# Optimization experiments

Measured on AMD Instinct MI355X. Metric: run time of the kernel, lower is better.

Reference implementation:

```python
import jax, jax.numpy as jnp
import numpy as np

B, S, IN, H, BB, M = 256, 512, 64, 256, 256, 64


def _lecun_tanh(x):
    return 1.7159 * jnp.tanh(0.666 * x)


def setup_inputs() -> dict:
    key = jax.random.key(0)
    ks = jax.random.split(key, 32)
    def g(i, shape, fan_in):
        return jax.random.normal(ks[i], shape, jnp.float32) * (fan_in ** -0.5)
    return {
        "x": jax.random.normal(ks[0], (B, S, IN), jnp.float32),
        "timespans": jax.random.uniform(ks[1], (B, S), jnp.float32, minval=0.01, maxval=1.0),
        "hx": jnp.zeros((B, H), jnp.float32),
        # CfC cell backbone (2 layers, lecun_tanh)
        "bb_w0": g(2, (IN + H, BB), IN + H), "bb_b0": jnp.zeros((BB,), jnp.float32),
        "bb_w1": g(3, (BB, BB), BB), "bb_b1": jnp.zeros((BB,), jnp.float32),
        # CfC heads ff1/ff2/time_a/time_b
        "ff1_w": g(4, (BB, H), BB), "ff1_b": jnp.zeros((H,), jnp.float32),
        "ff2_w": g(5, (BB, H), BB), "ff2_b": jnp.zeros((H,), jnp.float32),
        "ta_w": g(6, (BB, H), BB), "ta_b": jnp.zeros((H,), jnp.float32),
        "tb_w": g(7, (BB, H), BB), "tb_b": jnp.zeros((H,), jnp.float32),
        # projection hidden -> motor
        "proj_w": g(8, (H, M), H), "proj_b": jnp.zeros((M,), jnp.float32),
        # intensity head: M->16 SiLU ->3 Softplus
        "ih_w0": g(9, (M, 16), M), "ih_b0": jnp.zeros((16,), jnp.float32),
        "ih_w1": g(10, (16, 3), 16), "ih_b1": jnp.zeros((3,), jnp.float32),
        # action head: M->16 SiLU ->1 Tanh
        "ah_w0": g(11, (M, 16), M), "ah_b0": jnp.zeros((16,), jnp.float32),
        "ah_w1": g(12, (16, 1), 16), "ah_b1": jnp.zeros((1,), jnp.float32),
        # confidence head: M->8 SiLU ->1 Sigmoid
        "ch_w0": g(13, (M, 8), M), "ch_b0": jnp.zeros((8,), jnp.float32),
        "ch_w1": g(14, (8, 1), 8), "ch_b1": jnp.zeros((1,), jnp.float32),
    }


def reference(x, timespans, hx, bb_w0, bb_b0, bb_w1, bb_b1, ff1_w, ff1_b, ff2_w, ff2_b,
              ta_w, ta_b, tb_w, tb_b, proj_w, proj_b,
              ih_w0, ih_b0, ih_w1, ih_b1, ah_w0, ah_b0, ah_w1, ah_b1,
              ch_w0, ch_b0, ch_w1, ch_b1):
    ts = timespans[..., None]  # (B,S,1)

    def step(h, inp):
        x_t, ts_t = inp  # (B,IN), (B,1)
        z = jnp.concatenate([x_t, h], axis=-1)
        z = _lecun_tanh(z @ bb_w0 + bb_b0)
        z = _lecun_tanh(z @ bb_w1 + bb_b1)
        ff1 = jnp.tanh(z @ ff1_w + ff1_b)
        ff2 = jnp.tanh(z @ ff2_w + ff2_b)
        t_interp = jax.nn.sigmoid((z @ ta_w + ta_b) * ts_t + (z @ tb_w + tb_b))
        h_new = ff1 * (1.0 - t_interp) + t_interp * ff2
        return h_new, h_new

    xs = (jnp.swapaxes(x, 0, 1), jnp.swapaxes(ts, 0, 1))  # time-major
    h_n, h_seq = jax.lax.scan(step, hx, xs)               # h_seq: (S,B,H)
    cfc = jnp.swapaxes(h_seq, 0, 1) @ proj_w + proj_b     # (B,S,M)
    intensities = jax.nn.softplus(jax.nn.silu(cfc @ ih_w0 + ih_b0) @ ih_w1 + ih_b1)
    actions = jnp.tanh(jax.nn.silu(cfc @ ah_w0 + ah_b0) @ ah_w1 + ah_b1)
    confidence = jax.nn.sigmoid(jax.nn.silu(cfc @ ch_w0 + ch_b0) @ ch_w1 + ch_b1)
    return intensities, actions, confidence, h_n
```

## Files before the change

### kernel.cpp

```cpp
#include <hip/hip_runtime.h>
#include <hip/hip_bf16.h>

#define BN  256
#define SN  512
#define INN 64
#define HN  256
#define MN  64

#define ZINS 328
#define ZBS  264
#define CFS  72
#define HTS  36

#define OFF_ACT  393216
#define OFF_CONF 524288
#define OFF_HN   655360

#define FLAG_STRIDE 32
#define FLAG_BYTES  16384

typedef _Float16 h8 __attribute__((ext_vector_type(8)));
typedef float fx4 __attribute__((ext_vector_type(4)));
typedef unsigned long long u64;

union h4u {
    _Float16 h[4];
    u64 u;
};

__device__ __forceinline__ fx4 mfma16(h8 a, h8 b, fx4 c) {
    return __builtin_amdgcn_mfma_f32_16x16x32_f16(a, b, c, 0, 0, 0);
}
__device__ __forceinline__ float fast_tanh(float x) {
    float e = __expf(2.0f * x);
    return 1.0f - 2.0f / (e + 1.0f);
}
__device__ __forceinline__ float fast_sig(float x) { return 1.0f / (1.0f + __expf(-x)); }
__device__ __forceinline__ float lecun_tanh(float x) { return 1.7159f * fast_tanh(0.666f * x); }
__device__ __forceinline__ float softplus_f(float x) {
    return fmaxf(x, 0.0f) + __logf(1.0f + __expf(-fabsf(x)));
}

template <int NW>
__device__ __forceinline__ h8 loadB(const float* __restrict__ w, int col, int kbase) {
    h8 r;
#pragma unroll
    for (int j = 0; j < 8; ++j) r[j] = (_Float16)w[(kbase + j) * NW + col];
    return r;
}

__global__ void __launch_bounds__(512, 1) lh_scan_kernel(
    const float* __restrict__ x, const float* __restrict__ tsp, const float* __restrict__ hx,
    const float* __restrict__ w0, const float* __restrict__ b0,
    const float* __restrict__ w1, const float* __restrict__ b1,
    const float* __restrict__ f1w, const float* __restrict__ f1b,
    const float* __restrict__ f2w, const float* __restrict__ f2b,
    const float* __restrict__ taw, const float* __restrict__ tab,
    const float* __restrict__ tbw, const float* __restrict__ tbb,
    const float* __restrict__ pw, const float* __restrict__ pbias,
    const float* __restrict__ ihw0, const float* __restrict__ ihb0,
    const float* __restrict__ ihw1, const float* __restrict__ ihb1,
    const float* __restrict__ ahw0, const float* __restrict__ ahb0,
    const float* __restrict__ ahw1, const float* __restrict__ ahb1,
    const float* __restrict__ chw0, const float* __restrict__ chb0,
    const float* __restrict__ chw1, const float* __restrict__ chb1,
    float* __restrict__ out, unsigned int* __restrict__ flags,
    u64* __restrict__ hbuf)
{
    __shared__ __align__(16) _Float16 zin[16 * ZINS];
    __shared__ __align__(16) _Float16 z0b[16 * ZBS];
    __shared__ __align__(16) _Float16 z1b[16 * ZBS];
    __shared__ __align__(16) _Float16 cfcb[16 * CFS];
    __shared__ __align__(16) _Float16 pfl[8 * 4 * 64 * 8];
    __shared__ __align__(16) _Float16 w1l[8 * 8 * 64 * 8];
    __shared__ __align__(16) float htmp[4 * 16 * HTS];
    __shared__ float hidI[16 * 16];
    __shared__ float hidA[16 * 16];
    __shared__ float hidC[16 * 8];
    __shared__ float tsb[2][16];
    __shared__ float wsm[80];

    const int tid  = threadIdx.x;
    const int wv   = tid >> 6;
    const int lane = tid & 63;
    const int lo   = lane & 15;
    const int hi   = lane >> 4;
    const int hi8  = hi * 8;

    const int bid   = blockIdx.x;
    const int xcd   = bid & 7;
    const int c     = (bid >> 3) & 7;
    const int gsel  = bid >> 6;
    const int g     = xcd + 8 * gsel;
    const int bg    = g * 16;
    const int sbase = c * 32;

    if (tid < 48)          wsm[tid] = ihw1[tid];
    else if (tid < 51)     wsm[tid] = ihb1[tid - 48];
    else if (tid < 67)     wsm[tid] = ahw1[tid - 51];
    else if (tid == 67)    wsm[67]  = ahb1[0];
    else if (tid < 76)     wsm[tid] = chw1[tid - 68];
    else if (tid == 76)    wsm[76]  = chb1[0];

    {
        int r = tid >> 5, c8 = (tid & 31) * 8;
#pragma unroll
        for (int j = 0; j < 8; ++j)
            zin[r * ZINS + 64 + c8 + j] = (_Float16)hx[(bg + r) * HN + c8 + j];
        int c2 = (tid & 31) * 2;
        const float* xp = &x[((size_t)(bg + r) * SN + 0) * INN + c2];
        zin[r * ZINS + c2]     = (_Float16)xp[0];
        zin[r * ZINS + c2 + 1] = (_Float16)xp[1];
    }
    if (tid < 16) tsb[0][tid] = tsp[(bg + tid) * SN + 0];

    const int cg0 = wv, cg1 = wv + 8;
    const float b00 = b0[cg0 * 16 + lo], b01 = b0[cg1 * 16 + lo];
    const float b10 = b1[cg0 * 16 + lo], b11 = b1[cg1 * 16 + lo];

    const int hm  = wv >> 1;
    const int hcol = sbase + (wv & 1) * 16 + lo;
    const float* hwp = (hm == 0) ? f1w : (hm == 1) ? f2w : (hm == 2) ? taw : tbw;
    const float* hbp = (hm == 0) ? f1b : (hm == 1) ? f2b : (hm == 2) ? tab : tbb;
    const float hb = hbp[hcol];

    h8 w0f0[10], w0f1[10], w1f0[8], hdf[8];
#pragma unroll
    for (int kk = 0; kk < 10; ++kk) {
        w0f0[kk] = loadB<256>(w0, cg0 * 16 + lo, kk * 32 + hi8);
        w0f1[kk] = loadB<256>(w0, cg1 * 16 + lo, kk * 32 + hi8);
    }
#pragma unroll
    for (int kk = 0; kk < 8; ++kk) {
        w1f0[kk] = loadB<256>(w1, cg0 * 16 + lo, kk * 32 + hi8);
        hdf[kk]  = loadB<256>(hwp, hcol, kk * 32 + hi8);
        h8 f = loadB<256>(w1, cg1 * 16 + lo, kk * 32 + hi8);
        *(h8*)&w1l[((kk * 8 + wv) * 64 + lane) * 8] = f;
    }
    float pbv = 0.0f;
    if (wv < 4) {
        pbv = pbias[wv * 16 + lo];
#pragma unroll
        for (int kk = 0; kk < 8; ++kk) {
            h8 f = loadB<64>(pw, wv * 16 + lo, kk * 32 + hi8);
            *(h8*)&pfl[((kk * 4 + wv) * 64 + lane) * 8] = f;
        }
    }
    h8 hwf[2] = {};
    float hbv = 0.0f;
    if (wv == 4) {
        hbv = ihb0[lo];
#pragma unroll
        for (int kk = 0; kk < 2; ++kk) hwf[kk] = loadB<16>(ihw0, lo, kk * 32 + hi8);
    } else if (wv == 5) {
        hbv = ahb0[lo];
#pragma unroll
        for (int kk = 0; kk < 2; ++kk) hwf[kk] = loadB<16>(ahw0, lo, kk * 32 + hi8);
    } else if (wv == 6) {
        int cc = (lo < 8) ? lo : 0;
        hbv = (lo < 8) ? chb0[lo] : 0.0f;
#pragma unroll
        for (int kk = 0; kk < 2; ++kk) hwf[kk] = loadB<8>(chw0, cc, kk * 32 + hi8);
    }

    __syncthreads();

    for (int t = 0; t <= SN; ++t) {
        const int pr = t & 7;

        if (t < SN) {
            fx4 a0 = {b00, b00, b00, b00}, a1 = {b01, b01, b01, b01};
#pragma unroll
            for (int kk = 0; kk < 10; ++kk) {
                h8 a = *(const h8*)&zin[lo * ZINS + kk * 32 + hi8];
                a0 = mfma16(a, w0f0[kk], a0);
                a1 = mfma16(a, w0f1[kk], a1);
            }
#pragma unroll
            for (int i = 0; i < 4; ++i) {
                int r = hi * 4 + i;
                z0b[r * ZBS + cg0 * 16 + lo] = (_Float16)lecun_tanh(a0[i]);
                z0b[r * ZBS + cg1 * 16 + lo] = (_Float16)lecun_tanh(a1[i]);
            }
        }
        __syncthreads();

        if (t + 1 < SN) {
            int r = tid >> 5, c2 = (tid & 31) * 2;
            const float* xp = &x[((size_t)(bg + r) * SN + (t + 1)) * INN + c2];
            zin[r * ZINS + c2]     = (_Float16)xp[0];
            zin[r * ZINS + c2 + 1] = (_Float16)xp[1];
            if (tid < 16) tsb[(t + 1) & 1][tid] = tsp[(bg + tid) * SN + t + 1];
        }

        if (t < SN) {
            fx4 a0 = {b10, b10, b10, b10}, a1 = {b11, b11, b11, b11};
#pragma unroll
            for (int kk = 0; kk < 8; ++kk) {
                h8 a = *(const h8*)&z0b[lo * ZBS + kk * 32 + hi8];
                h8 b1f = *(const h8*)&w1l[((kk * 8 + wv) * 64 + lane) * 8];
                a0 = mfma16(a, w1f0[kk], a0);
                a1 = mfma16(a, b1f, a1);
            }
#pragma unroll
            for (int i = 0; i < 4; ++i) {
                int r = hi * 4 + i;
                z1b[r * ZBS + cg0 * 16 + lo] = (_Float16)lecun_tanh(a0[i]);
                z1b[r * ZBS + cg1 * 16 + lo] = (_Float16)lecun_tanh(a1[i]);
            }
        }
        __syncthreads();

        if (t < SN) {
            fx4 acc = {hb, hb, hb, hb};
#pragma unroll
            for (int kk = 0; kk < 8; ++kk) {
                h8 a = *(const h8*)&z1b[lo * ZBS + kk * 32 + hi8];
                acc = mfma16(a, hdf[kk], acc);
            }
#pragma unroll
            for (int i = 0; i < 4; ++i)
                htmp[(hm * 16 + hi * 4 + i) * HTS + (wv & 1) * 16 + lo] = acc[i];
        }
        __syncthreads();

        if (t < SN && tid < 128) {
            int r = tid >> 3, c4 = (tid & 7) * 4;
            h4u pk;
            float hn3 = 0.0f;
#pragma unroll
            for (int k = 0; k < 4; ++k) {
                float a1v = htmp[(0 * 16 + r) * HTS + c4 + k];
                float a2v = htmp[(1 * 16 + r) * HTS + c4 + k];
                float a3v = htmp[(2 * 16 + r) * HTS + c4 + k];
                float a4v = htmp[(3 * 16 + r) * HTS + c4 + k];
                float tv  = tsb[t & 1][r];
                float ff1 = fast_tanh(a1v);
                float ff2 = fast_tanh(a2v);
                float ti  = fast_sig(a3v * tv + a4v);
                float hn  = ff1 + ti * (ff2 - ff1);
                pk.h[k] = (_Float16)hn;
                if (t == SN - 1) out[OFF_HN + (bg + r) * HN + sbase + c4 + k] = hn;
                hn3 = hn;
            }
            (void)hn3;
            size_t idx = ((((size_t)((t + 1) & 1) * 16 + g) * 16) + r) * 64 + (sbase + c4) / 4;
            __hip_atomic_store(&hbuf[idx], pk.u, __ATOMIC_RELAXED, __HIP_MEMORY_SCOPE_AGENT);
        }
        __syncthreads();
        if (t < SN && tid == 0)
            __hip_atomic_store(&flags[(g * 8 + c) * FLAG_STRIDE], (unsigned)(t + 1),
                               __ATOMIC_RELAXED, __HIP_MEMORY_SCOPE_AGENT);

        if (t >= 1 && c == pr && wv < 4) {
            fx4 acc = {pbv, pbv, pbv, pbv};
#pragma unroll
            for (int kk = 0; kk < 8; ++kk) {
                h8 a = *(const h8*)&zin[lo * ZINS + 64 + kk * 32 + hi8];
                h8 b = *(const h8*)&pfl[((kk * 4 + wv) * 64 + lane) * 8];
                acc = mfma16(a, b, acc);
            }
#pragma unroll
            for (int i = 0; i < 4; ++i)
                cfcb[(hi * 4 + i) * CFS + wv * 16 + lo] = (_Float16)acc[i];
        }
        __syncthreads();

        if (t >= 1 && c == pr && wv >= 4 && wv < 7) {
            fx4 acc = {hbv, hbv, hbv, hbv};
#pragma unroll
            for (int kk = 0; kk < 2; ++kk) {
                h8 a = *(const h8*)&cfcb[lo * CFS + kk * 32 + hi8];
                acc = mfma16(a, hwf[kk], acc);
            }
#pragma unroll
            for (int i = 0; i < 4; ++i) {
                float v = acc[i];
                v = v * fast_sig(v);
                int r = hi * 4 + i;
                if (wv == 4)       hidI[r * 16 + lo] = v;
                else if (wv == 5)  hidA[r * 16 + lo] = v;
                else if (lo < 8)   hidC[r * 8 + lo]  = v;
            }
        }
        __syncthreads();

        if (t >= 1 && c == pr && tid < 80) {
            int r = tid / 5, o = tid % 5;
            int tc = t - 1;
            int b = bg + r;
            if (o < 3) {
                float s = wsm[48 + o];
#pragma unroll
                for (int u = 0; u < 16; ++u) s += hidI[r * 16 + u] * wsm[u * 3 + o];
                out[(size_t)(b * SN + tc) * 3 + o] = softplus_f(s);
            } else if (o == 3) {
                float s = wsm[67];
#pragma unroll
                for (int u = 0; u < 16; ++u) s += hidA[r * 16 + u] * wsm[51 + u];
                out[OFF_ACT + b * SN + tc] = fast_tanh(s);
            } else {
                float s = wsm[76];
#pragma unroll
                for (int u = 0; u < 8; ++u) s += hidC[r * 8 + u] * wsm[68 + u];
                out[OFF_CONF + b * SN + tc] = fast_sig(s);
            }
        }

        if (t < SN) {
            if (tid < 8) {
                unsigned target = (unsigned)(t + 1);
                while (__hip_atomic_load(&flags[(g * 8 + tid) * FLAG_STRIDE],
                                         __ATOMIC_RELAXED, __HIP_MEMORY_SCOPE_AGENT) < target) {}
            }
            __syncthreads();
            {
                int r = tid >> 5, c8 = (tid & 31) * 8;
                size_t idx = ((((size_t)((t + 1) & 1) * 16 + g) * 16) + r) * 64 + c8 / 4;
                u64 v0 = __hip_atomic_load(&hbuf[idx],     __ATOMIC_RELAXED, __HIP_MEMORY_SCOPE_AGENT);
                u64 v1 = __hip_atomic_load(&hbuf[idx + 1], __ATOMIC_RELAXED, __HIP_MEMORY_SCOPE_AGENT);
                *(u64*)&zin[r * ZINS + 64 + c8]     = v0;
                *(u64*)&zin[r * ZINS + 64 + c8 + 4] = v1;
            }
        }
        __syncthreads();
    }
}

extern "C" void kernel_launch(void* const* d_in, const int* in_sizes, int n_in,
                              void* d_out, int out_size, void* d_ws, size_t ws_size,
                              hipStream_t stream) {
    (void)in_sizes; (void)n_in; (void)out_size; (void)ws_size;
    const float* p[29];
    for (int i = 0; i < 29; ++i) p[i] = (const float*)d_in[i];
    unsigned int* flags = (unsigned int*)d_ws;
    u64* hbuf = (u64*)((char*)d_ws + FLAG_BYTES);
    hipMemsetAsync(d_ws, 0, FLAG_BYTES, stream);
    hipLaunchKernelGGL(lh_scan_kernel, dim3(128), dim3(512), 0, stream,
        p[0], p[1], p[2], p[3], p[4], p[5], p[6], p[7], p[8], p[9], p[10], p[11], p[12],
        p[13], p[14], p[15], p[16], p[17], p[18], p[19], p[20], p[21], p[22], p[23],
        p[24], p[25], p[26], p[27], p[28], (float*)d_out, flags, hbuf);
}
```

Before: 2.325 ms.

## Double block to 1024 threads, one column group per wave, overlap projection

```diff
diff --git a/kernel.cpp b/kernel.cpp
--- a/kernel.cpp
+++ b/kernel.cpp
@@ -22,11 +22,7 @@
 typedef _Float16 h8 __attribute__((ext_vector_type(8)));
 typedef float fx4 __attribute__((ext_vector_type(4)));
 typedef unsigned long long u64;
-
-union h4u {
-    _Float16 h[4];
-    u64 u;
-};
+union h4u { _Float16 h[4]; u64 u; };
 
 __device__ __forceinline__ fx4 mfma16(h8 a, h8 b, fx4 c) {
     return __builtin_amdgcn_mfma_f32_16x16x32_f16(a, b, c, 0, 0, 0);
@@ -49,7 +45,7 @@
     return r;
 }
 
-__global__ void __launch_bounds__(512, 1) lh_scan_kernel(
+__global__ void __launch_bounds__(1024, 1) lh_scan_kernel(
     const float* __restrict__ x, const float* __restrict__ tsp, const float* __restrict__ hx,
     const float* __restrict__ w0, const float* __restrict__ b0,
     const float* __restrict__ w1, const float* __restrict__ b1,
@@ -71,8 +67,8 @@
     __shared__ __align__(16) _Float16 z0b[16 * ZBS];
     __shared__ __align__(16) _Float16 z1b[16 * ZBS];
     __shared__ __align__(16) _Float16 cfcb[16 * CFS];
+    __shared__ __align__(16) _Float16 hdl[8 * 8 * 64 * 8];
     __shared__ __align__(16) _Float16 pfl[8 * 4 * 64 * 8];
-    __shared__ __align__(16) _Float16 w1l[8 * 8 * 64 * 8];
     __shared__ __align__(16) float htmp[4 * 16 * HTS];
     __shared__ float hidI[16 * 16];
     __shared__ float hidA[16 * 16];
@@ -102,7 +98,7 @@
     else if (tid < 76)     wsm[tid] = chw1[tid - 68];
     else if (tid == 76)    wsm[76]  = chb1[0];
 
-    {
+    if (tid < 512) {
         int r = tid >> 5, c8 = (tid & 31) * 8;
 #pragma unroll
         for (int j = 0; j < 8; ++j)
@@ -114,49 +110,49 @@
     }
     if (tid < 16) tsb[0][tid] = tsp[(bg + tid) * SN + 0];
 
-    const int cg0 = wv, cg1 = wv + 8;
-    const float b00 = b0[cg0 * 16 + lo], b01 = b0[cg1 * 16 + lo];
-    const float b10 = b1[cg0 * 16 + lo], b11 = b1[cg1 * 16 + lo];
-
-    const int hm  = wv >> 1;
+    const float b0v = b0[wv * 16 + lo];
+    const float b1v = b1[wv * 16 + lo];
+
+    h8 w0f[10], w1f[8];
+#pragma unroll
+    for (int kk = 0; kk < 10; ++kk) w0f[kk] = loadB<256>(w0, wv * 16 + lo, kk * 32 + hi8);
+#pragma unroll
+    for (int kk = 0; kk < 8; ++kk)  w1f[kk] = loadB<256>(w1, wv * 16 + lo, kk * 32 + hi8);
+
+    const int hm   = wv >> 1;
     const int hcol = sbase + (wv & 1) * 16 + lo;
-    const float* hwp = (hm == 0) ? f1w : (hm == 1) ? f2w : (hm == 2) ? taw : tbw;
-    const float* hbp = (hm == 0) ? f1b : (hm == 1) ? f2b : (hm == 2) ? tab : tbb;
-    const float hb = hbp[hcol];
-
-    h8 w0f0[10], w0f1[10], w1f0[8], hdf[8];
-#pragma unroll
-    for (int kk = 0; kk < 10; ++kk) {
-        w0f0[kk] = loadB<256>(w0, cg0 * 16 + lo, kk * 32 + hi8);
-        w0f1[kk] = loadB<256>(w0, cg1 * 16 + lo, kk * 32 + hi8);
-    }
-#pragma unroll
-    for (int kk = 0; kk < 8; ++kk) {
-        w1f0[kk] = loadB<256>(w1, cg0 * 16 + lo, kk * 32 + hi8);
-        hdf[kk]  = loadB<256>(hwp, hcol, kk * 32 + hi8);
-        h8 f = loadB<256>(w1, cg1 * 16 + lo, kk * 32 + hi8);
-        *(h8*)&w1l[((kk * 8 + wv) * 64 + lane) * 8] = f;
+    float hb = 0.0f;
+    if (wv < 8) {
+        const float* hwp = (hm == 0) ? f1w : (hm == 1) ? f2w : (hm == 2) ? taw : tbw;
+        const float* hbp = (hm == 0) ? f1b : (hm == 1) ? f2b : (hm == 2) ? tab : tbb;
+        hb = hbp[hcol];
+#pragma unroll
+        for (int kk = 0; kk < 8; ++kk) {
+            h8 f = loadB<256>(hwp, hcol, kk * 32 + hi8);
+            *(h8*)&hdl[((wv * 8 + kk) * 64 + lane) * 8] = f;
+        }
     }
     float pbv = 0.0f;
-    if (wv < 4) {
-        pbv = pbias[wv * 16 + lo];
+    if (wv >= 8 && wv < 12) {
+        int u = wv - 8;
+        pbv = pbias[u * 16 + lo];
 #pragma unroll
         for (int kk = 0; kk < 8; ++kk) {
-            h8 f = loadB<64>(pw, wv * 16 + lo, kk * 32 + hi8);
-            *(h8*)&pfl[((kk * 4 + wv) * 64 + lane) * 8] = f;
+            h8 f = loadB<64>(pw, u * 16 + lo, kk * 32 + hi8);
+            *(h8*)&pfl[((kk * 4 + u) * 64 + lane) * 8] = f;
         }
     }
     h8 hwf[2] = {};
     float hbv = 0.0f;
-    if (wv == 4) {
+    if (wv == 12) {
         hbv = ihb0[lo];
 #pragma unroll
         for (int kk = 0; kk < 2; ++kk) hwf[kk] = loadB<16>(ihw0, lo, kk * 32 + hi8);
-    } else if (wv == 5) {
+    } else if (wv == 13) {
         hbv = ahb0[lo];
 #pragma unroll
         for (int kk = 0; kk < 2; ++kk) hwf[kk] = loadB<16>(ahw0, lo, kk * 32 + hi8);
-    } else if (wv == 6) {
+    } else if (wv == 14) {
         int cc = (lo < 8) ? lo : 0;
         hbv = (lo < 8) ? chb0[lo] : 0.0f;
 #pragma unroll
@@ -169,23 +165,19 @@
         const int pr = t & 7;
 
         if (t < SN) {
-            fx4 a0 = {b00, b00, b00, b00}, a1 = {b01, b01, b01, b01};
+            fx4 acc = {b0v, b0v, b0v, b0v};
 #pragma unroll
             for (int kk = 0; kk < 10; ++kk) {
                 h8 a = *(const h8*)&zin[lo * ZINS + kk * 32 + hi8];
-                a0 = mfma16(a, w0f0[kk], a0);
-                a1 = mfma16(a, w0f1[kk], a1);
-            }
-#pragma unroll
-            for (int i = 0; i < 4; ++i) {
-                int r = hi * 4 + i;
-                z0b[r * ZBS + cg0 * 16 + lo] = (_Float16)lecun_tanh(a0[i]);
-                z0b[r * ZBS + cg1 * 16 + lo] = (_Float16)lecun_tanh(a1[i]);
-            }
-        }
-        __syncthreads();
-
-        if (t + 1 < SN) {
+                acc = mfma16(a, w0f[kk], acc);
+            }
+#pragma unroll
+            for (int i = 0; i < 4; ++i)
+                z0b[(hi * 4 + i) * ZBS + wv * 16 + lo] = (_Float16)lecun_tanh(acc[i]);
+        }
+        __syncthreads();
+
+        if (t + 1 < SN && tid < 512) {
             int r = tid >> 5, c2 = (tid & 31) * 2;
             const float* xp = &x[((size_t)(bg + r) * SN + (t + 1)) * INN + c2];
             zin[r * ZINS + c2]     = (_Float16)xp[0];
@@ -194,40 +186,48 @@
         }
 
         if (t < SN) {
-            fx4 a0 = {b10, b10, b10, b10}, a1 = {b11, b11, b11, b11};
+            fx4 acc = {b1v, b1v, b1v, b1v};
 #pragma unroll
             for (int kk = 0; kk < 8; ++kk) {
                 h8 a = *(const h8*)&z0b[lo * ZBS + kk * 32 + hi8];
-                h8 b1f = *(const h8*)&w1l[((kk * 8 + wv) * 64 + lane) * 8];
-                a0 = mfma16(a, w1f0[kk], a0);
-                a1 = mfma16(a, b1f, a1);
-            }
-#pragma unroll
-            for (int i = 0; i < 4; ++i) {
-                int r = hi * 4 + i;
-                z1b[r * ZBS + cg0 * 16 + lo] = (_Float16)lecun_tanh(a0[i]);
-                z1b[r * ZBS + cg1 * 16 + lo] = (_Float16)lecun_tanh(a1[i]);
-            }
-        }
-        __syncthreads();
-
-        if (t < SN) {
+                acc = mfma16(a, w1f[kk], acc);
+            }
+#pragma unroll
+            for (int i = 0; i < 4; ++i)
+                z1b[(hi * 4 + i) * ZBS + wv * 16 + lo] = (_Float16)lecun_tanh(acc[i]);
+        }
+        __syncthreads();
+
+        if (t < SN && wv < 8) {
             fx4 acc = {hb, hb, hb, hb};
 #pragma unroll
             for (int kk = 0; kk < 8; ++kk) {
                 h8 a = *(const h8*)&z1b[lo * ZBS + kk * 32 + hi8];
-                acc = mfma16(a, hdf[kk], acc);
+                h8 b = *(const h8*)&hdl[((wv * 8 + kk) * 64 + lane) * 8];
+                acc = mfma16(a, b, acc);
             }
 #pragma unroll
             for (int i = 0; i < 4; ++i)
                 htmp[(hm * 16 + hi * 4 + i) * HTS + (wv & 1) * 16 + lo] = acc[i];
+        }
+        if (t >= 1 && c == pr && wv >= 8 && wv < 12) {
+            int u = wv - 8;
+            fx4 acc = {pbv, pbv, pbv, pbv};
+#pragma unroll
+            for (int kk = 0; kk < 8; ++kk) {
+                h8 a = *(const h8*)&zin[lo * ZINS + 64 + kk * 32 + hi8];
+                h8 b = *(const h8*)&pfl[((kk * 4 + u) * 64 + lane) * 8];
+                acc = mfma16(a, b, acc);
+            }
+#pragma unroll
+            for (int i = 0; i < 4; ++i)
+                cfcb[(hi * 4 + i) * CFS + u * 16 + lo] = (_Float16)acc[i];
         }
         __syncthreads();
 
         if (t < SN && tid < 128) {
             int r = tid >> 3, c4 = (tid & 7) * 4;
             h4u pk;
-            float hn3 = 0.0f;
 #pragma unroll
             for (int k = 0; k < 4; ++k) {
                 float a1v = htmp[(0 * 16 + r) * HTS + c4 + k];
@@ -241,32 +241,11 @@
                 float hn  = ff1 + ti * (ff2 - ff1);
                 pk.h[k] = (_Float16)hn;
                 if (t == SN - 1) out[OFF_HN + (bg + r) * HN + sbase + c4 + k] = hn;
-                hn3 = hn;
-            }
-            (void)hn3;
-            size_t idx = ((((size_t)((t + 1) & 1) * 16 + g) * 16) + r) * 64 + (sbase + c4) / 4;
+            }
+            size_t idx = (((size_t)((t + 1) & 1) * 256) + g * 16 + r) * 64 + (sbase + c4) / 4;
             __hip_atomic_store(&hbuf[idx], pk.u, __ATOMIC_RELAXED, __HIP_MEMORY_SCOPE_AGENT);
         }
-        __syncthreads();
-        if (t < SN && tid == 0)
-            __hip_atomic_store(&flags[(g * 8 + c) * FLAG_STRIDE], (unsigned)(t + 1),
-                               __ATOMIC_RELAXED, __HIP_MEMORY_SCOPE_AGENT);
-
-        if (t >= 1 && c == pr && wv < 4) {
-            fx4 acc = {pbv, pbv, pbv, pbv};
-#pragma unroll
-            for (int kk = 0; kk < 8; ++kk) {
-                h8 a = *(const h8*)&zin[lo * ZINS + 64 + kk * 32 + hi8];
-                h8 b = *(const h8*)&pfl[((kk * 4 + wv) * 64 + lane) * 8];
-                acc = mfma16(a, b, acc);
-            }
-#pragma unroll
-            for (int i = 0; i < 4; ++i)
-                cfcb[(hi * 4 + i) * CFS + wv * 16 + lo] = (_Float16)acc[i];
-        }
-        __syncthreads();
-
-        if (t >= 1 && c == pr && wv >= 4 && wv < 7) {
+        if (t >= 1 && c == pr && wv >= 12 && wv < 15) {
             fx4 acc = {hbv, hbv, hbv, hbv};
 #pragma unroll
             for (int kk = 0; kk < 2; ++kk) {
@@ -278,15 +257,19 @@
                 float v = acc[i];
                 v = v * fast_sig(v);
                 int r = hi * 4 + i;
-                if (wv == 4)       hidI[r * 16 + lo] = v;
-                else if (wv == 5)  hidA[r * 16 + lo] = v;
+                if (wv == 12)      hidI[r * 16 + lo] = v;
+                else if (wv == 13) hidA[r * 16 + lo] = v;
                 else if (lo < 8)   hidC[r * 8 + lo]  = v;
             }
         }
         __syncthreads();
-
-        if (t >= 1 && c == pr && tid < 80) {
-            int r = tid / 5, o = tid % 5;
+        if (t < SN && tid == 0)
+            __hip_atomic_store(&flags[(g * 8 + c) * FLAG_STRIDE], (unsigned)(t + 1),
+                               __ATOMIC_RELAXED, __HIP_MEMORY_SCOPE_AGENT);
+
+        if (t >= 1 && c == pr && tid >= 512 && tid < 592) {
+            int local = tid - 512;
+            int r = local / 5, o = local % 5;
             int tc = t - 1;
             int b = bg + r;
             if (o < 3) {
@@ -306,7 +289,6 @@
                 out[OFF_CONF + b * SN + tc] = fast_sig(s);
             }
         }
-
         if (t < SN) {
             if (tid < 8) {
                 unsigned target = (unsigned)(t + 1);
@@ -314,9 +296,9 @@
                                          __ATOMIC_RELAXED, __HIP_MEMORY_SCOPE_AGENT) < target) {}
             }
             __syncthreads();
-            {
+            if (tid < 512) {
                 int r = tid >> 5, c8 = (tid & 31) * 8;
-                size_t idx = ((((size_t)((t + 1) & 1) * 16 + g) * 16) + r) * 64 + c8 / 4;
+                size_t idx = (((size_t)((t + 1) & 1) * 256) + g * 16 + r) * 64 + c8 / 4;
                 u64 v0 = __hip_atomic_load(&hbuf[idx],     __ATOMIC_RELAXED, __HIP_MEMORY_SCOPE_AGENT);
                 u64 v1 = __hip_atomic_load(&hbuf[idx + 1], __ATOMIC_RELAXED, __HIP_MEMORY_SCOPE_AGENT);
                 *(u64*)&zin[r * ZINS + 64 + c8]     = v0;
@@ -336,7 +318,7 @@
     unsigned int* flags = (unsigned int*)d_ws;
     u64* hbuf = (u64*)((char*)d_ws + FLAG_BYTES);
     hipMemsetAsync(d_ws, 0, FLAG_BYTES, stream);
-    hipLaunchKernelGGL(lh_scan_kernel, dim3(128), dim3(512), 0, stream,
+    hipLaunchKernelGGL(lh_scan_kernel, dim3(128), dim3(1024), 0, stream,
         p[0], p[1], p[2], p[3], p[4], p[5], p[6], p[7], p[8], p[9], p[10], p[11], p[12],
         p[13], p[14], p[15], p[16], p[17], p[18], p[19], p[20], p[21], p[22], p[23],
         p[24], p[25], p[26], p[27], p[28], (float*)d_out, flags, hbuf);
```

Measured after the change: 3.125 ms. 1.34x slower.

## Halve block to four waves, keep all weights in registers, merge step barriers

Applied to the files above, without the earlier changes.

```diff
diff --git a/kernel.cpp b/kernel.cpp
--- a/kernel.cpp
+++ b/kernel.cpp
@@ -22,11 +22,7 @@
 typedef _Float16 h8 __attribute__((ext_vector_type(8)));
 typedef float fx4 __attribute__((ext_vector_type(4)));
 typedef unsigned long long u64;
-
-union h4u {
-    _Float16 h[4];
-    u64 u;
-};
+union h4u { _Float16 h[4]; u64 u; };
 
 __device__ __forceinline__ fx4 mfma16(h8 a, h8 b, fx4 c) {
     return __builtin_amdgcn_mfma_f32_16x16x32_f16(a, b, c, 0, 0, 0);
@@ -49,7 +45,7 @@
     return r;
 }
 
-__global__ void __launch_bounds__(512, 1) lh_scan_kernel(
+__global__ void __launch_bounds__(256, 1) lh_scan_kernel(
     const float* __restrict__ x, const float* __restrict__ tsp, const float* __restrict__ hx,
     const float* __restrict__ w0, const float* __restrict__ b0,
     const float* __restrict__ w1, const float* __restrict__ b1,
@@ -72,7 +68,6 @@
     __shared__ __align__(16) _Float16 z1b[16 * ZBS];
     __shared__ __align__(16) _Float16 cfcb[16 * CFS];
     __shared__ __align__(16) _Float16 pfl[8 * 4 * 64 * 8];
-    __shared__ __align__(16) _Float16 w1l[8 * 8 * 64 * 8];
     __shared__ __align__(16) float htmp[4 * 16 * HTS];
     __shared__ float hidI[16 * 16];
     __shared__ float hidA[16 * 16];
@@ -103,60 +98,69 @@
     else if (tid == 76)    wsm[76]  = chb1[0];
 
     {
-        int r = tid >> 5, c8 = (tid & 31) * 8;
-#pragma unroll
-        for (int j = 0; j < 8; ++j)
-            zin[r * ZINS + 64 + c8 + j] = (_Float16)hx[(bg + r) * HN + c8 + j];
-        int c2 = (tid & 31) * 2;
-        const float* xp = &x[((size_t)(bg + r) * SN + 0) * INN + c2];
-        zin[r * ZINS + c2]     = (_Float16)xp[0];
-        zin[r * ZINS + c2 + 1] = (_Float16)xp[1];
+        int r = tid >> 4, c16 = (tid & 15) * 16;
+#pragma unroll
+        for (int j = 0; j < 16; ++j)
+            zin[r * ZINS + 64 + c16 + j] = (_Float16)hx[(bg + r) * HN + c16 + j];
+        int c4 = (tid & 15) * 4;
+        fx4 xv = *(const fx4*)&x[((size_t)(bg + r) * SN + 0) * INN + c4];
+        h4u pk;
+#pragma unroll
+        for (int j = 0; j < 4; ++j) pk.h[j] = (_Float16)xv[j];
+        *(u64*)&zin[r * ZINS + c4] = pk.u;
     }
     if (tid < 16) tsb[0][tid] = tsp[(bg + tid) * SN + 0];
 
-    const int cg0 = wv, cg1 = wv + 8;
-    const float b00 = b0[cg0 * 16 + lo], b01 = b0[cg1 * 16 + lo];
-    const float b10 = b1[cg0 * 16 + lo], b11 = b1[cg1 * 16 + lo];
-
-    const int hm  = wv >> 1;
-    const int hcol = sbase + (wv & 1) * 16 + lo;
-    const float* hwp = (hm == 0) ? f1w : (hm == 1) ? f2w : (hm == 2) ? taw : tbw;
-    const float* hbp = (hm == 0) ? f1b : (hm == 1) ? f2b : (hm == 2) ? tab : tbb;
-    const float hb = hbp[hcol];
-
-    h8 w0f0[10], w0f1[10], w1f0[8], hdf[8];
-#pragma unroll
-    for (int kk = 0; kk < 10; ++kk) {
-        w0f0[kk] = loadB<256>(w0, cg0 * 16 + lo, kk * 32 + hi8);
-        w0f1[kk] = loadB<256>(w0, cg1 * 16 + lo, kk * 32 + hi8);
-    }
-#pragma unroll
-    for (int kk = 0; kk < 8; ++kk) {
-        w1f0[kk] = loadB<256>(w1, cg0 * 16 + lo, kk * 32 + hi8);
-        hdf[kk]  = loadB<256>(hwp, hcol, kk * 32 + hi8);
-        h8 f = loadB<256>(w1, cg1 * 16 + lo, kk * 32 + hi8);
-        *(h8*)&w1l[((kk * 8 + wv) * 64 + lane) * 8] = f;
-    }
-    float pbv = 0.0f;
-    if (wv < 4) {
-        pbv = pbias[wv * 16 + lo];
+    float b0v[4], b1v[4];
+#pragma unroll
+    for (int q = 0; q < 4; ++q) {
+        b0v[q] = b0[(wv * 4 + q) * 16 + lo];
+        b1v[q] = b1[(wv * 4 + q) * 16 + lo];
+    }
+
+    const float* hwp = (wv == 0) ? f1w : (wv == 1) ? f2w : (wv == 2) ? taw : tbw;
+    const float* hbp = (wv == 0) ? f1b : (wv == 1) ? f2b : (wv == 2) ? tab : tbb;
+    float hbs[2] = { hbp[sbase + lo], hbp[sbase + 16 + lo] };
+
+    h8 w0f[4][10], w1f[4][8], hdf[2][8];
+#pragma unroll
+    for (int q = 0; q < 4; ++q) {
+#pragma unroll
+        for (int kk = 0; kk < 10; ++kk)
+            w0f[q][kk] = loadB<256>(w0, (wv * 4 + q) * 16 + lo, kk * 32 + hi8);
+#pragma unroll
+        for (int kk = 0; kk < 8; ++kk)
+            w1f[q][kk] = loadB<256>(w1, (wv * 4 + q) * 16 + lo, kk * 32 + hi8);
+    }
+#pragma unroll
+    for (int s = 0; s < 2; ++s)
+#pragma unroll
+        for (int kk = 0; kk < 8; ++kk)
+            hdf[s][kk] = loadB<256>(hwp, sbase + s * 16 + lo, kk * 32 + hi8);
+
+    {
 #pragma unroll
         for (int kk = 0; kk < 8; ++kk) {
             h8 f = loadB<64>(pw, wv * 16 + lo, kk * 32 + hi8);
             *(h8*)&pfl[((kk * 4 + wv) * 64 + lane) * 8] = f;
         }
     }
+    float pbv[2] = { 0.0f, 0.0f };
+    if (wv >= 2) {
+        pbv[0] = pbias[((wv - 2) * 2 + 0) * 16 + lo];
+        pbv[1] = pbias[((wv - 2) * 2 + 1) * 16 + lo];
+    }
     h8 hwf[2] = {};
     float hbv = 0.0f;
-    if (wv == 4) {
+    if (wv == 0) {
         hbv = ihb0[lo];
 #pragma unroll
         for (int kk = 0; kk < 2; ++kk) hwf[kk] = loadB<16>(ihw0, lo, kk * 32 + hi8);
-    } else if (wv == 5) {
+    } else if (wv == 1) {
         hbv = ahb0[lo];
 #pragma unroll
         for (int kk = 0; kk < 2; ++kk) hwf[kk] = loadB<16>(ahw0, lo, kk * 32 + hi8);
-    } else if (wv == 6) {
+    } else if (wv == 2) {
         int cc = (lo < 8) ? lo : 0;
         hbv = (lo < 8) ? chb0[lo] : 0.0f;
 #pragma unroll
@@ -169,104 +173,123 @@
         const int pr = t & 7;
 
         if (t < SN) {
-            fx4 a0 = {b00, b00, b00, b00}, a1 = {b01, b01, b01, b01};
+            fx4 a0 = {b0v[0], b0v[0], b0v[0], b0v[0]};
+            fx4 a1 = {b0v[1], b0v[1], b0v[1], b0v[1]};
+            fx4 a2 = {b0v[2], b0v[2], b0v[2], b0v[2]};
+            fx4 a3 = {b0v[3], b0v[3], b0v[3], b0v[3]};
 #pragma unroll
             for (int kk = 0; kk < 10; ++kk) {
                 h8 a = *(const h8*)&zin[lo * ZINS + kk * 32 + hi8];
-                a0 = mfma16(a, w0f0[kk], a0);
-                a1 = mfma16(a, w0f1[kk], a1);
+                a0 = mfma16(a, w0f[0][kk], a0);
+                a1 = mfma16(a, w0f[1][kk], a1);
+                a2 = mfma16(a, w0f[2][kk], a2);
+                a3 = mfma16(a, w0f[3][kk], a3);
             }
 #pragma unroll
             for (int i = 0; i < 4; ++i) {
                 int r = hi * 4 + i;
-                z0b[r * ZBS + cg0 * 16 + lo] = (_Float16)lecun_tanh(a0[i]);
-                z0b[r * ZBS + cg1 * 16 + lo] = (_Float16)lecun_tanh(a1[i]);
+                z0b[r * ZBS + (wv * 4 + 0) * 16 + lo] = (_Float16)lecun_tanh(a0[i]);
+                z0b[r * ZBS + (wv * 4 + 1) * 16 + lo] = (_Float16)lecun_tanh(a1[i]);
+                z0b[r * ZBS + (wv * 4 + 2) * 16 + lo] = (_Float16)lecun_tanh(a2[i]);
+                z0b[r * ZBS + (wv * 4 + 3) * 16 + lo] = (_Float16)lecun_tanh(a3[i]);
             }
         }
         __syncthreads();
 
         if (t + 1 < SN) {
-            int r = tid >> 5, c2 = (tid & 31) * 2;
-            const float* xp = &x[((size_t)(bg + r) * SN + (t + 1)) * INN + c2];
-            zin[r * ZINS + c2]     = (_Float16)xp[0];
-            zin[r * ZINS + c2 + 1] = (_Float16)xp[1];
+            int r = tid >> 4, c4 = (tid & 15) * 4;
+            fx4 xv = *(const fx4*)&x[((size_t)(bg + r) * SN + (t + 1)) * INN + c4];
+            h4u pk;
+#pragma unroll
+            for (int j = 0; j < 4; ++j) pk.h[j] = (_Float16)xv[j];
+            *(u64*)&zin[r * ZINS + c4] = pk.u;
             if (tid < 16) tsb[(t + 1) & 1][tid] = tsp[(bg + tid) * SN + t + 1];
         }
-
         if (t < SN) {
-            fx4 a0 = {b10, b10, b10, b10}, a1 = {b11, b11, b11, b11};
+            fx4 a0 = {b1v[0], b1v[0], b1v[0], b1v[0]};
+            fx4 a1 = {b1v[1], b1v[1], b1v[1], b1v[1]};
+            fx4 a2 = {b1v[2], b1v[2], b1v[2], b1v[2]};
+            fx4 a3 = {b1v[3], b1v[3], b1v[3], b1v[3]};
 #pragma unroll
             for (int kk = 0; kk < 8; ++kk) {
                 h8 a = *(const h8*)&z0b[lo * ZBS + kk * 32 + hi8];
-                h8 b1f = *(const h8*)&w1l[((kk * 8 + wv) * 64 + lane) * 8];
-                a0 = mfma16(a, w1f0[kk], a0);
-                a1 = mfma16(a, b1f, a1);
+                a0 = mfma16(a, w1f[0][kk], a0);
+                a1 = mfma16(a, w1f[1][kk], a1);
+                a2 = mfma16(a, w1f[2][kk], a2);
+                a3 = mfma16(a, w1f[3][kk], a3);
             }
 #pragma unroll
             for (int i = 0; i < 4; ++i) {
                 int r = hi * 4 + i;
-                z1b[r * ZBS + cg0 * 16 + lo] = (_Float16)lecun_tanh(a0[i]);
-                z1b[r * ZBS + cg1 * 16 + lo] = (_Float16)lecun_tanh(a1[i]);
+                z1b[r * ZBS + (wv * 4 + 0) * 16 + lo] = (_Float16)lecun_tanh(a0[i]);
+                z1b[r * ZBS + (wv * 4 + 1) * 16 + lo] = (_Float16)lecun_tanh(a1[i]);
+                z1b[r * ZBS + (wv * 4 + 2) * 16 + lo] = (_Float16)lecun_tanh(a2[i]);
+                z1b[r * ZBS + (wv * 4 + 3) * 16 + lo] = (_Float16)lecun_tanh(a3[i]);
             }
         }
         __syncthreads();
 
         if (t < SN) {
-            fx4 acc = {hb, hb, hb, hb};
+            fx4 a0 = {hbs[0], hbs[0], hbs[0], hbs[0]};
+            fx4 a1 = {hbs[1], hbs[1], hbs[1], hbs[1]};
 #pragma unroll
             for (int kk = 0; kk < 8; ++kk) {
                 h8 a = *(const h8*)&z1b[lo * ZBS + kk * 32 + hi8];
-                acc = mfma16(a, hdf[kk], acc);
-            }
-#pragma unroll
-            for (int i = 0; i < 4; ++i)
-                htmp[(hm * 16 + hi * 4 + i) * HTS + (wv & 1) * 16 + lo] = acc[i];
+                a0 = mfma16(a, hdf[0][kk], a0);
+                a1 = mfma16(a, hdf[1][kk], a1);
+            }
+#pragma unroll
+            for (int i = 0; i < 4; ++i) {
+                htmp[(wv * 16 + hi * 4 + i) * HTS + lo]      = a0[i];
+                htmp[(wv * 16 + hi * 4 + i) * HTS + 16 + lo] = a1[i];
+            }
         }
         __syncthreads();
 
         if (t < SN && tid < 128) {
             int r = tid >> 3, c4 = (tid & 7) * 4;
+            fx4 v0 = *(const fx4*)&htmp[(0 * 16 + r) * HTS + c4];
+            fx4 v1 = *(const fx4*)&htmp[(1 * 16 + r) * HTS + c4];
+            fx4 v2 = *(const fx4*)&htmp[(2 * 16 + r) * HTS + c4];
+            fx4 v3 = *(const fx4*)&htmp[(3 * 16 + r) * HTS + c4];
+            float tv = tsb[t & 1][r];
             h4u pk;
-            float hn3 = 0.0f;
 #pragma unroll
             for (int k = 0; k < 4; ++k) {
-                float a1v = htmp[(0 * 16 + r) * HTS + c4 + k];
-                float a2v = htmp[(1 * 16 + r) * HTS + c4 + k];
-                float a3v = htmp[(2 * 16 + r) * HTS + c4 + k];
-                float a4v = htmp[(3 * 16 + r) * HTS + c4 + k];
-                float tv  = tsb[t & 1][r];
-                float ff1 = fast_tanh(a1v);
-                float ff2 = fast_tanh(a2v);
-                float ti  = fast_sig(a3v * tv + a4v);
+                float ff1 = fast_tanh(v0[k]);
+                float ff2 = fast_tanh(v1[k]);
+                float ti  = fast_sig(v2[k] * tv + v3[k]);
                 float hn  = ff1 + ti * (ff2 - ff1);
                 pk.h[k] = (_Float16)hn;
                 if (t == SN - 1) out[OFF_HN + (bg + r) * HN + sbase + c4 + k] = hn;
-                hn3 = hn;
-            }
-            (void)hn3;
-            size_t idx = ((((size_t)((t + 1) & 1) * 16 + g) * 16) + r) * 64 + (sbase + c4) / 4;
+            }
+            size_t idx = (((size_t)((t + 1) & 1) * 256) + g * 16 + r) * 64 + (sbase + c4) / 4;
             __hip_atomic_store(&hbuf[idx], pk.u, __ATOMIC_RELAXED, __HIP_MEMORY_SCOPE_AGENT);
         }
-        __syncthreads();
-        if (t < SN && tid == 0)
-            __hip_atomic_store(&flags[(g * 8 + c) * FLAG_STRIDE], (unsigned)(t + 1),
-                               __ATOMIC_RELAXED, __HIP_MEMORY_SCOPE_AGENT);
-
-        if (t >= 1 && c == pr && wv < 4) {
-            fx4 acc = {pbv, pbv, pbv, pbv};
+        if (t >= 1 && c == pr && wv >= 2) {
+            fx4 a0 = {pbv[0], pbv[0], pbv[0], pbv[0]};
+            fx4 a1 = {pbv[1], pbv[1], pbv[1], pbv[1]};
+            int cg0 = (wv - 2) * 2, cg1 = cg0 + 1;
 #pragma unroll
             for (int kk = 0; kk < 8; ++kk) {
                 h8 a = *(const h8*)&zin[lo * ZINS + 64 + kk * 32 + hi8];
-                h8 b = *(const h8*)&pfl[((kk * 4 + wv) * 64 + lane) * 8];
-                acc = mfma16(a, b, acc);
-            }
-#pragma unroll
-            for (int i = 0; i < 4; ++i)
-                cfcb[(hi * 4 + i) * CFS + wv * 16 + lo] = (_Float16)acc[i];
-        }
-        __syncthreads();
-
-        if (t >= 1 && c == pr && wv >= 4 && wv < 7) {
+                h8 f0 = *(const h8*)&pfl[((kk * 4 + cg0) * 64 + lane) * 8];
+                h8 f1 = *(const h8*)&pfl[((kk * 4 + cg1) * 64 + lane) * 8];
+                a0 = mfma16(a, f0, a0);
+                a1 = mfma16(a, f1, a1);
+            }
+#pragma unroll
+            for (int i = 0; i < 4; ++i) {
+                cfcb[(hi * 4 + i) * CFS + cg0 * 16 + lo] = (_Float16)a0[i];
+                cfcb[(hi * 4 + i) * CFS + cg1 * 16 + lo] = (_Float16)a1[i];
+            }
+        }
+        __syncthreads();
+        if (t < SN && tid == 0)
+            __hip_atomic_store(&flags[(g * 8 + c) * FLAG_STRIDE], (unsigned)(t + 2),
+                               __ATOMIC_RELAXED, __HIP_MEMORY_SCOPE_AGENT);
+
+        if (t >= 1 && c == pr && wv < 3) {
             fx4 acc = {hbv, hbv, hbv, hbv};
 #pragma unroll
             for (int kk = 0; kk < 2; ++kk) {
@@ -278,49 +301,69 @@
                 float v = acc[i];
                 v = v * fast_sig(v);
                 int r = hi * 4 + i;
-                if (wv == 4)       hidI[r * 16 + lo] = v;
-                else if (wv == 5)  hidA[r * 16 + lo] = v;
+                if (wv == 0)       hidI[r * 16 + lo] = v;
+                else if (wv == 1)  hidA[r * 16 + lo] = v;
                 else if (lo < 8)   hidC[r * 8 + lo]  = v;
             }
         }
-        __syncthreads();
-
-        if (t >= 1 && c == pr && tid < 80) {
-            int r = tid / 5, o = tid % 5;
+        if (t < SN && wv == 3 && lane < 8) {
+            unsigned target = (unsigned)(t + 2);
+            while (__hip_atomic_load(&flags[(g * 8 + lane) * FLAG_STRIDE],
+                                     __ATOMIC_RELAXED, __HIP_MEMORY_SCOPE_AGENT) < target) {}
+        }
+        __syncthreads();
+
+        if (t < SN) {
+            int r = tid >> 4, cw = (tid & 15) * 16;
+            size_t idx = (((size_t)((t + 1) & 1) * 256) + g * 16 + r) * 64 + cw / 4;
+            u64 v0 = __hip_atomic_load(&hbuf[idx],     __ATOMIC_RELAXED, __HIP_MEMORY_SCOPE_AGENT);
+            u64 v1 = __hip_atomic_load(&hbuf[idx + 1], __ATOMIC_RELAXED, __HIP_MEMORY_SCOPE_AGENT);
+            u64 v2 = __hip_atomic_load(&hbuf[idx + 2], __ATOMIC_RELAXED, __HIP_MEMORY_SCOPE_AGENT);
+            u64 v3 = __hip_atomic_load(&hbuf[idx + 3], __ATOMIC_RELAXED, __HIP_MEMORY_SCOPE_AGENT);
+            if (t >= 1 && c == pr && tid < 80) {
+                int rr = tid / 5, o = tid % 5;
+                int tc = t - 1;
+                int b = bg + rr;
+                if (o < 3) {
+                    float s = wsm[48 + o];
+#pragma unroll
+                    for (int u = 0; u < 16; ++u) s += hidI[rr * 16 + u] * wsm[u * 3 + o];
+                    out[(size_t)(b * SN + tc) * 3 + o] = softplus_f(s);
+                } else if (o == 3) {
+                    float s = wsm[67];
+#pragma unroll
+                    for (int u = 0; u < 16; ++u) s += hidA[rr * 16 + u] * wsm[51 + u];
+                    out[OFF_ACT + b * SN + tc] = fast_tanh(s);
+                } else {
+                    float s = wsm[76];
+#pragma unroll
+                    for (int u = 0; u < 8; ++u) s += hidC[rr * 8 + u] * wsm[68 + u];
+                    out[OFF_CONF + b * SN + tc] = fast_sig(s);
+                }
+            }
+            *(u64*)&zin[r * ZINS + 64 + cw]      = v0;
+            *(u64*)&zin[r * ZINS + 64 + cw + 4]  = v1;
+            *(u64*)&zin[r * ZINS + 64 + cw + 8]  = v2;
+            *(u64*)&zin[r * ZINS + 64 + cw + 12] = v3;
+        } else if (t >= 1 && c == pr && tid < 80) {
+            int rr = tid / 5, o = tid % 5;
             int tc = t - 1;
-            int b = bg + r;
+            int b = bg + rr;
             if (o < 3) {
                 float s = wsm[48 + o];
 #pragma unroll
-                for (int u = 0; u < 16; ++u) s += hidI[r * 16 + u] * wsm[u * 3 + o];
+                for (int u = 0; u < 16; ++u) s += hidI[rr * 16 + u] * wsm[u * 3 + o];
                 out[(size_t)(b * SN + tc) * 3 + o] = softplus_f(s);
             } else if (o == 3) {
                 float s = wsm[67];
 #pragma unroll
-                for (int u = 0; u < 16; ++u) s += hidA[r * 16 + u] * wsm[51 + u];
+                for (int u = 0; u < 16; ++u) s += hidA[rr * 16 + u] * wsm[51 + u];
                 out[OFF_ACT + b * SN + tc] = fast_tanh(s);
             } else {
                 float s = wsm[76];
 #pragma unroll
-                for (int u = 0; u < 8; ++u) s += hidC[r * 8 + u] * wsm[68 + u];
+                for (int u = 0; u < 8; ++u) s += hidC[rr * 8 + u] * wsm[68 + u];
                 out[OFF_CONF + b * SN + tc] = fast_sig(s);
-            }
-        }
-
-        if (t < SN) {
-            if (tid < 8) {
-                unsigned target = (unsigned)(t + 1);
-                while (__hip_atomic_load(&flags[(g * 8 + tid) * FLAG_STRIDE],
-                                         __ATOMIC_RELAXED, __HIP_MEMORY_SCOPE_AGENT) < target) {}
-            }
-            __syncthreads();
-            {
-                int r = tid >> 5, c8 = (tid & 31) * 8;
-                size_t idx = ((((size_t)((t + 1) & 1) * 16 + g) * 16) + r) * 64 + c8 / 4;
-                u64 v0 = __hip_atomic_load(&hbuf[idx],     __ATOMIC_RELAXED, __HIP_MEMORY_SCOPE_AGENT);
-                u64 v1 = __hip_atomic_load(&hbuf[idx + 1], __ATOMIC_RELAXED, __HIP_MEMORY_SCOPE_AGENT);
-                *(u64*)&zin[r * ZINS + 64 + c8]     = v0;
-                *(u64*)&zin[r * ZINS + 64 + c8 + 4] = v1;
             }
         }
         __syncthreads();
@@ -336,7 +379,7 @@
     unsigned int* flags = (unsigned int*)d_ws;
     u64* hbuf = (u64*)((char*)d_ws + FLAG_BYTES);
     hipMemsetAsync(d_ws, 0, FLAG_BYTES, stream);
-    hipLaunchKernelGGL(lh_scan_kernel, dim3(128), dim3(512), 0, stream,
+    hipLaunchKernelGGL(lh_scan_kernel, dim3(128), dim3(256), 0, stream,
         p[0], p[1], p[2], p[3], p[4], p[5], p[6], p[7], p[8], p[9], p[10], p[11], p[12],
         p[13], p[14], p[15], p[16], p[17], p[18], p[19], p[20], p[21], p[22], p[23],
         p[24], p[25], p[26], p[27], p[28], (float*)d_out, flags, hbuf);
```

New measurement: 2.818 ms. +21.2%, slower.

## Cut barriers per step and overlap x-part GEMM with cross-block h exchange

Applied to the files above, without the earlier changes.

```diff
diff --git a/kernel.cpp b/kernel.cpp
--- a/kernel.cpp
+++ b/kernel.cpp
@@ -22,11 +22,7 @@
 typedef _Float16 h8 __attribute__((ext_vector_type(8)));
 typedef float fx4 __attribute__((ext_vector_type(4)));
 typedef unsigned long long u64;
-
-union h4u {
-    _Float16 h[4];
-    u64 u;
-};
+union h4u { _Float16 h[4]; u64 u; };
 
 __device__ __forceinline__ fx4 mfma16(h8 a, h8 b, fx4 c) {
     return __builtin_amdgcn_mfma_f32_16x16x32_f16(a, b, c, 0, 0, 0);
@@ -118,7 +114,7 @@
     const float b00 = b0[cg0 * 16 + lo], b01 = b0[cg1 * 16 + lo];
     const float b10 = b1[cg0 * 16 + lo], b11 = b1[cg1 * 16 + lo];
 
-    const int hm  = wv >> 1;
+    const int hm   = wv >> 1;
     const int hcol = sbase + (wv & 1) * 16 + lo;
     const float* hwp = (hm == 0) ? f1w : (hm == 1) ? f2w : (hm == 2) ? taw : tbw;
     const float* hbp = (hm == 0) ? f1b : (hm == 1) ? f2b : (hm == 2) ? tab : tbb;
@@ -137,26 +133,26 @@
         h8 f = loadB<256>(w1, cg1 * 16 + lo, kk * 32 + hi8);
         *(h8*)&w1l[((kk * 8 + wv) * 64 + lane) * 8] = f;
     }
-    float pbv = 0.0f;
     if (wv < 4) {
-        pbv = pbias[wv * 16 + lo];
 #pragma unroll
         for (int kk = 0; kk < 8; ++kk) {
             h8 f = loadB<64>(pw, wv * 16 + lo, kk * 32 + hi8);
             *(h8*)&pfl[((kk * 4 + wv) * 64 + lane) * 8] = f;
         }
     }
+    float pbv = 0.0f;
+    if (wv >= 2 && wv < 6) pbv = pbias[(wv - 2) * 16 + lo];
     h8 hwf[2] = {};
     float hbv = 0.0f;
-    if (wv == 4) {
+    if (wv == 2) {
         hbv = ihb0[lo];
 #pragma unroll
         for (int kk = 0; kk < 2; ++kk) hwf[kk] = loadB<16>(ihw0, lo, kk * 32 + hi8);
-    } else if (wv == 5) {
+    } else if (wv == 3) {
         hbv = ahb0[lo];
 #pragma unroll
         for (int kk = 0; kk < 2; ++kk) hwf[kk] = loadB<16>(ahw0, lo, kk * 32 + hi8);
-    } else if (wv == 6) {
+    } else if (wv == 4) {
         int cc = (lo < 8) ? lo : 0;
         hbv = (lo < 8) ? chb0[lo] : 0.0f;
 #pragma unroll
@@ -165,16 +161,24 @@
 
     __syncthreads();
 
+    fx4 zx0 = {b00, b00, b00, b00}, zx1 = {b01, b01, b01, b01};
+    {
+        h8 ax0 = *(const h8*)&zin[lo * ZINS + 0 * 32 + hi8];
+        h8 ax1 = *(const h8*)&zin[lo * ZINS + 1 * 32 + hi8];
+        zx0 = mfma16(ax0, w0f0[0], zx0); zx1 = mfma16(ax0, w0f1[0], zx1);
+        zx0 = mfma16(ax1, w0f0[1], zx0); zx1 = mfma16(ax1, w0f1[1], zx1);
+    }
+
     for (int t = 0; t <= SN; ++t) {
         const int pr = t & 7;
 
         if (t < SN) {
-            fx4 a0 = {b00, b00, b00, b00}, a1 = {b01, b01, b01, b01};
-#pragma unroll
-            for (int kk = 0; kk < 10; ++kk) {
-                h8 a = *(const h8*)&zin[lo * ZINS + kk * 32 + hi8];
-                a0 = mfma16(a, w0f0[kk], a0);
-                a1 = mfma16(a, w0f1[kk], a1);
+            fx4 a0 = zx0, a1 = zx1;
+#pragma unroll
+            for (int j = 0; j < 8; ++j) {
+                h8 a = *(const h8*)&zin[lo * ZINS + 64 + j * 32 + hi8];
+                a0 = mfma16(a, w0f0[j + 2], a0);
+                a1 = mfma16(a, w0f1[j + 2], a1);
             }
 #pragma unroll
             for (int i = 0; i < 4; ++i) {
@@ -192,15 +196,14 @@
             zin[r * ZINS + c2 + 1] = (_Float16)xp[1];
             if (tid < 16) tsb[(t + 1) & 1][tid] = tsp[(bg + tid) * SN + t + 1];
         }
-
         if (t < SN) {
             fx4 a0 = {b10, b10, b10, b10}, a1 = {b11, b11, b11, b11};
 #pragma unroll
             for (int kk = 0; kk < 8; ++kk) {
                 h8 a = *(const h8*)&z0b[lo * ZBS + kk * 32 + hi8];
-                h8 b1f = *(const h8*)&w1l[((kk * 8 + wv) * 64 + lane) * 8];
+                h8 bf = *(const h8*)&w1l[((kk * 8 + wv) * 64 + lane) * 8];
                 a0 = mfma16(a, w1f0[kk], a0);
-                a1 = mfma16(a, b1f, a1);
+                a1 = mfma16(a, bf, a1);
             }
 #pragma unroll
             for (int i = 0; i < 4; ++i) {
@@ -226,47 +229,43 @@
 
         if (t < SN && tid < 128) {
             int r = tid >> 3, c4 = (tid & 7) * 4;
+            fx4 v0 = *(const fx4*)&htmp[(0 * 16 + r) * HTS + c4];
+            fx4 v1 = *(const fx4*)&htmp[(1 * 16 + r) * HTS + c4];
+            fx4 v2 = *(const fx4*)&htmp[(2 * 16 + r) * HTS + c4];
+            fx4 v3 = *(const fx4*)&htmp[(3 * 16 + r) * HTS + c4];
+            float tv = tsb[t & 1][r];
             h4u pk;
-            float hn3 = 0.0f;
 #pragma unroll
             for (int k = 0; k < 4; ++k) {
-                float a1v = htmp[(0 * 16 + r) * HTS + c4 + k];
-                float a2v = htmp[(1 * 16 + r) * HTS + c4 + k];
-                float a3v = htmp[(2 * 16 + r) * HTS + c4 + k];
-                float a4v = htmp[(3 * 16 + r) * HTS + c4 + k];
-                float tv  = tsb[t & 1][r];
-                float ff1 = fast_tanh(a1v);
-                float ff2 = fast_tanh(a2v);
-                float ti  = fast_sig(a3v * tv + a4v);
+                float ff1 = fast_tanh(v0[k]);
+                float ff2 = fast_tanh(v1[k]);
+                float ti  = fast_sig(v2[k] * tv + v3[k]);
                 float hn  = ff1 + ti * (ff2 - ff1);
                 pk.h[k] = (_Float16)hn;
                 if (t == SN - 1) out[OFF_HN + (bg + r) * HN + sbase + c4 + k] = hn;
-                hn3 = hn;
-            }
-            (void)hn3;
-            size_t idx = ((((size_t)((t + 1) & 1) * 16 + g) * 16) + r) * 64 + (sbase + c4) / 4;
+            }
+            size_t idx = (((size_t)((t + 1) & 1) * 256) + g * 16 + r) * 64 + (sbase + c4) / 4;
             __hip_atomic_store(&hbuf[idx], pk.u, __ATOMIC_RELAXED, __HIP_MEMORY_SCOPE_AGENT);
+        }
+        if (t >= 1 && c == pr && wv >= 2 && wv < 6) {
+            int u = wv - 2;
+            fx4 acc = {pbv, pbv, pbv, pbv};
+#pragma unroll
+            for (int kk = 0; kk < 8; ++kk) {
+                h8 a = *(const h8*)&zin[lo * ZINS + 64 + kk * 32 + hi8];
+                h8 b = *(const h8*)&pfl[((kk * 4 + u) * 64 + lane) * 8];
+                acc = mfma16(a, b, acc);
+            }
+#pragma unroll
+            for (int i = 0; i < 4; ++i)
+                cfcb[(hi * 4 + i) * CFS + u * 16 + lo] = (_Float16)acc[i];
         }
         __syncthreads();
         if (t < SN && tid == 0)
             __hip_atomic_store(&flags[(g * 8 + c) * FLAG_STRIDE], (unsigned)(t + 1),
                                __ATOMIC_RELAXED, __HIP_MEMORY_SCOPE_AGENT);
 
-        if (t >= 1 && c == pr && wv < 4) {
-            fx4 acc = {pbv, pbv, pbv, pbv};
-#pragma unroll
-            for (int kk = 0; kk < 8; ++kk) {
-                h8 a = *(const h8*)&zin[lo * ZINS + 64 + kk * 32 + hi8];
-                h8 b = *(const h8*)&pfl[((kk * 4 + wv) * 64 + lane) * 8];
-                acc = mfma16(a, b, acc);
-            }
-#pragma unroll
-            for (int i = 0; i < 4; ++i)
-                cfcb[(hi * 4 + i) * CFS + wv * 16 + lo] = (_Float16)acc[i];
-        }
-        __syncthreads();
-
-        if (t >= 1 && c == pr && wv >= 4 && wv < 7) {
+        if (t >= 1 && c == pr && wv >= 2 && wv < 5) {
             fx4 acc = {hbv, hbv, hbv, hbv};
 #pragma unroll
             for (int kk = 0; kk < 2; ++kk) {
@@ -278,50 +277,58 @@
                 float v = acc[i];
                 v = v * fast_sig(v);
                 int r = hi * 4 + i;
-                if (wv == 4)       hidI[r * 16 + lo] = v;
-                else if (wv == 5)  hidA[r * 16 + lo] = v;
+                if (wv == 2)       hidI[r * 16 + lo] = v;
+                else if (wv == 3)  hidA[r * 16 + lo] = v;
                 else if (lo < 8)   hidC[r * 8 + lo]  = v;
             }
         }
-        __syncthreads();
-
-        if (t >= 1 && c == pr && tid < 80) {
-            int r = tid / 5, o = tid % 5;
+        if (t < SN && wv == 7 && lane < 8) {
+            unsigned target = (unsigned)(t + 1);
+            while (__hip_atomic_load(&flags[(g * 8 + lane) * FLAG_STRIDE],
+                                     __ATOMIC_RELAXED, __HIP_MEMORY_SCOPE_AGENT) < target) {}
+        }
+        __syncthreads();
+
+        u64 v0 = 0, v1 = 0;
+        int lr = tid >> 5, lc8 = (tid & 31) * 8;
+        if (t < SN) {
+            size_t idx = (((size_t)((t + 1) & 1) * 256) + g * 16 + lr) * 64 + lc8 / 4;
+            v0 = __hip_atomic_load(&hbuf[idx],     __ATOMIC_RELAXED, __HIP_MEMORY_SCOPE_AGENT);
+            v1 = __hip_atomic_load(&hbuf[idx + 1], __ATOMIC_RELAXED, __HIP_MEMORY_SCOPE_AGENT);
+        }
+        zx0 = fx4{b00, b00, b00, b00};
+        zx1 = fx4{b01, b01, b01, b01};
+        if (t + 1 < SN) {
+            h8 ax0 = *(const h8*)&zin[lo * ZINS + 0 * 32 + hi8];
+            h8 ax1 = *(const h8*)&zin[lo * ZINS + 1 * 32 + hi8];
+            zx0 = mfma16(ax0, w0f0[0], zx0); zx1 = mfma16(ax0, w0f1[0], zx1);
+            zx0 = mfma16(ax1, w0f0[1], zx0); zx1 = mfma16(ax1, w0f1[1], zx1);
+        }
+        if (t >= 1 && c == pr && tid >= 384 && tid < 464) {
+            int local = tid - 384;
+            int rr = local / 5, o = local % 5;
             int tc = t - 1;
-            int b = bg + r;
+            int b = bg + rr;
             if (o < 3) {
                 float s = wsm[48 + o];
 #pragma unroll
-                for (int u = 0; u < 16; ++u) s += hidI[r * 16 + u] * wsm[u * 3 + o];
+                for (int u = 0; u < 16; ++u) s += hidI[rr * 16 + u] * wsm[u * 3 + o];
                 out[(size_t)(b * SN + tc) * 3 + o] = softplus_f(s);
             } else if (o == 3) {
                 float s = wsm[67];
 #pragma unroll
-                for (int u = 0; u < 16; ++u) s += hidA[r * 16 + u] * wsm[51 + u];
+                for (int u = 0; u < 16; ++u) s += hidA[rr * 16 + u] * wsm[51 + u];
                 out[OFF_ACT + b * SN + tc] = fast_tanh(s);
             } else {
                 float s = wsm[76];
 #pragma unroll
-                for (int u = 0; u < 8; ++u) s += hidC[r * 8 + u] * wsm[68 + u];
+                for (int u = 0; u < 8; ++u) s += hidC[rr * 8 + u] * wsm[68 + u];
                 out[OFF_CONF + b * SN + tc] = fast_sig(s);
             }
         }
-
-        if (t < SN) {
-            if (tid < 8) {
-                unsigned target = (unsigned)(t + 1);
-                while (__hip_atomic_load(&flags[(g * 8 + tid) * FLAG_STRIDE],
-                                         __ATOMIC_RELAXED, __HIP_MEMORY_SCOPE_AGENT) < target) {}
-            }
-            __syncthreads();
-            {
-                int r = tid >> 5, c8 = (tid & 31) * 8;
-                size_t idx = ((((size_t)((t + 1) & 1) * 16 + g) * 16) + r) * 64 + c8 / 4;
-                u64 v0 = __hip_atomic_load(&hbuf[idx],     __ATOMIC_RELAXED, __HIP_MEMORY_SCOPE_AGENT);
-                u64 v1 = __hip_atomic_load(&hbuf[idx + 1], __ATOMIC_RELAXED, __HIP_MEMORY_SCOPE_AGENT);
-                *(u64*)&zin[r * ZINS + 64 + c8]     = v0;
-                *(u64*)&zin[r * ZINS + 64 + c8 + 4] = v1;
-            }
+        if (t < SN) {
+            *(u64*)&zin[lr * ZINS + 64 + lc8]     = v0;
+            *(u64*)&zin[lr * ZINS + 64 + lc8 + 4] = v1;
         }
         __syncthreads();
     }
```

New measurement: 2.453 ms. +5.5%, slower.
